# Optimization experiments

Measured on AMD Instinct MI355X. Metric: run time of the kernel, lower is better.

Reference implementation:

```python
import jax, jax.numpy as jnp
import numpy as np

H, D = 6, 64          # num_heads, head_dim (embed_dim = 384)
WIN = 33              # window_size
PAD = (WIN - 1) // 2  # 16


def setup_inputs() -> dict:
    key = jax.random.key(0)
    ks = jax.random.split(key, 9)
    B, L, E = 8, 1025, 384
    s = 1.0 / np.sqrt(E).astype(np.float32)
    return {
        "x": jax.random.normal(ks[0], (B, L, E), jnp.float32),
        "Wq": jax.random.normal(ks[1], (E, E), jnp.float32) * s,
        "bq": jax.random.normal(ks[2], (E,), jnp.float32) * 0.01,
        "Wk": jax.random.normal(ks[3], (E, E), jnp.float32) * s,
        "bk": jax.random.normal(ks[4], (E,), jnp.float32) * 0.01,
        "Wv": jax.random.normal(ks[5], (E, E), jnp.float32) * s,
        "bv": jax.random.normal(ks[6], (E,), jnp.float32) * 0.01,
        "Wo": jax.random.normal(ks[7], (E, E), jnp.float32) * s,
        "bo": jax.random.normal(ks[8], (E,), jnp.float32) * 0.01,
    }


def reference(x, Wq, bq, Wk, bk, Wv, bv, Wo, bo):
    B, L, E = x.shape
    scale = 1.0 / np.sqrt(D).astype(np.float32)

    def proj(W, b):
        # (B,L,E) -> (B,H,L,D)
        return (x @ W + b).reshape(B, L, H, D).transpose(0, 2, 1, 3)

    Q, K, V = proj(Wq, bq), proj(Wk, bk), proj(Wv, bv)

    # --- cls token (position 0): full attention over all keys ---
    s_cls = jnp.einsum('bhqd,bhkd->bhqk', Q[:, :, :1], K) * scale
    out_cls = jnp.einsum('bhqk,bhkd->bhqd', jax.nn.softmax(s_cls, -1), V)

    # --- remaining tokens: local window + cls appended to every window ---
    Lr = L - 1
    pos = jnp.arange(1, L)                                    # absolute query pos (Lr,)
    idx = pos[:, None] + jnp.arange(WIN)[None, :] - PAD
    # original masks out-of-range AND the cls slot (abs pos 0) inside the window
    valid = (idx >= 1) & (idx < L)
    idxc = jnp.clip(idx, 0, L - 1)

    Kw = K[:, :, idxc]
    Vw = V[:, :, idxc]
    cls_k = jnp.broadcast_to(K[:, :, :1, None, :], (B, H, Lr, 1, D))
    cls_v = jnp.broadcast_to(V[:, :, :1, None, :], (B, H, Lr, 1, D))
    Kw = jnp.concatenate([Kw, cls_k], axis=3)
    Vw = jnp.concatenate([Vw, cls_v], axis=3)
    mask = jnp.concatenate([valid, jnp.ones((Lr, 1), bool)], axis=-1)

    s_rest = jnp.einsum('bhld,bhlwd->bhlw', Q[:, :, 1:], Kw) * scale
    s_rest = jnp.where(mask[None, None], s_rest, -jnp.inf)
    a_rest = jax.nn.softmax(s_rest, axis=-1)
    out_rest = jnp.einsum('bhlw,bhlwd->bhld', a_rest, Vw)

    out = jnp.concatenate([out_cls, out_rest], axis=2)        # (B,H,L,D)
    out = out.transpose(0, 2, 1, 3).reshape(B, L, E)
    return out @ Wo + bo
```

## Files before the change

kernel.cpp:

```cpp
#include <hip/hip_runtime.h>
#include <hip/hip_bf16.h>

typedef unsigned short ushort_t;
typedef __attribute__((ext_vector_type(8))) short short8;
typedef __attribute__((ext_vector_type(4))) float f32x4;

constexpr int Bc = 8;
constexpr int Lc = 1025;
constexpr int Ec = 384;
constexpr int Hc = 6;
constexpr int Dc = 64;
constexpr int MT = Bc * Lc;
constexpr int BHLD = Bc * Hc * Lc * Dc;
constexpr float SCALE = 0.125f;
constexpr int NCH = 5;

__device__ __forceinline__ float bf2f(ushort_t u) {
    union { unsigned int u; float f; } v; v.u = ((unsigned int)u) << 16; return v.f;
}
__device__ __forceinline__ ushort_t f2bf(float f) {
    union { float f; unsigned int u; } v; v.f = f;
    unsigned int r = v.u + 0x7FFFu + ((v.u >> 16) & 1u);
    return (ushort_t)(r >> 16);
}

#define GLOAD_LDS16(gp, lp)                                                          \
    __builtin_amdgcn_global_load_lds(                                                \
        (const __attribute__((address_space(1))) unsigned int*)(gp),                 \
        (__attribute__((address_space(3))) unsigned int*)(lp), 16, 0, 0)

__global__ __launch_bounds__(256) void prep_kernel(
    const float* __restrict__ x, ushort_t* __restrict__ xb,
    const float* __restrict__ Wq, const float* __restrict__ Wk,
    const float* __restrict__ Wv, const float* __restrict__ Wo,
    ushort_t* __restrict__ Wt_all)
{
    const int bid = blockIdx.x;
    if (bid < 3075) {
        int i = bid * 256 + threadIdx.x;
        float4 v = ((const float4*)x)[i];
        ushort4 o;
        o.x = f2bf(v.x); o.y = f2bf(v.y); o.z = f2bf(v.z); o.w = f2bf(v.w);
        ((ushort4*)xb)[i] = o;
        return;
    }
    __shared__ float t[32][33];
    const int b2 = bid - 3075;
    const int z = b2 / 144, rem = b2 - z * 144;
    const int yy = rem / 12, xx = rem - yy * 12;
    const float* W = (z == 0) ? Wq : (z == 1) ? Wk : (z == 2) ? Wv : Wo;
    ushort_t* Wt = Wt_all + (size_t)z * Ec * Ec;
    const int x0 = xx * 32, y0 = yy * 32;
    const int tx = threadIdx.x & 31, ty = threadIdx.x >> 5;
#pragma unroll
    for (int j = 0; j < 4; j++)
        t[ty + 8 * j][tx] = W[(size_t)(y0 + ty + 8 * j) * Ec + x0 + tx];
    __syncthreads();
#pragma unroll
    for (int j = 0; j < 4; j++)
        Wt[(size_t)(x0 + ty + 8 * j) * Ec + y0 + tx] = f2bf(t[tx][ty + 8 * j]);
}

__global__ __launch_bounds__(256) void qkv_mfma_kernel(
    const ushort_t* __restrict__ xb, const ushort_t* __restrict__ Wt,
    const float* __restrict__ bq, const float* __restrict__ bk,
    const float* __restrict__ bv, ushort_t* __restrict__ qkv)
{
    __shared__ __align__(16) ushort_t As[128 * 64];
    __shared__ __align__(16) ushort_t Bs[128 * 64];

    const int tid = threadIdx.x;
    const int lane = tid & 63;
    const int wid = tid >> 6;
    const int wr = wid >> 1, wc = wid & 1;
    const int m0 = blockIdx.x * 128;
    const int n0 = blockIdx.y * 128;
    const int which = n0 / Ec;
    const int nm0 = n0 - which * Ec;
    const ushort_t* Wmat = Wt + (size_t)which * Ec * Ec;
    const float* bias = (which == 0) ? bq : (which == 1) ? bk : bv;

    f32x4 acc[4][4];
#pragma unroll
    for (int i = 0; i < 4; i++)
#pragma unroll
        for (int j = 0; j < 4; j++) acc[i][j] = (f32x4){0.f, 0.f, 0.f, 0.f};

    for (int kt = 0; kt < Ec; kt += 64) {
#pragma unroll
        for (int c = 0; c < 4; c++) {
            int ci  = (wid * 4 + c) * 64 + lane;
            int row = ci >> 3, kc = ci & 7;
            int kcs = kc ^ (row & 7);
            int rowA = m0 + row; rowA = rowA < MT ? rowA : MT - 1;
            GLOAD_LDS16(xb + (size_t)rowA * Ec + kt + kcs * 8,
                        As + (size_t)(wid * 4 + c) * 512);
            GLOAD_LDS16(Wmat + (size_t)(nm0 + row) * Ec + kt + kcs * 8,
                        Bs + (size_t)(wid * 4 + c) * 512);
        }
        __syncthreads();

#pragma unroll
        for (int ki = 0; ki < 2; ki++) {
            short8 a[4], b[4];
            const int kchunk = ki * 4 + (lane >> 4);
#pragma unroll
            for (int mi = 0; mi < 4; mi++) {
                int row = wr * 64 + mi * 16 + (lane & 15);
                a[mi] = *(const short8*)(As + row * 64 + ((kchunk ^ (row & 7)) * 8));
            }
#pragma unroll
            for (int ni = 0; ni < 4; ni++) {
                int row = wc * 64 + ni * 16 + (lane & 15);
                b[ni] = *(const short8*)(Bs + row * 64 + ((kchunk ^ (row & 7)) * 8));
            }
#pragma unroll
            for (int mi = 0; mi < 4; mi++)
#pragma unroll
                for (int ni = 0; ni < 4; ni++)
                    acc[mi][ni] = __builtin_amdgcn_mfma_f32_16x16x32_bf16(
                        a[mi], b[ni], acc[mi][ni], 0, 0, 0);
        }
        __syncthreads();
    }

    const int colL = lane & 15;
    const int rowL = (lane >> 4) * 4;
#pragma unroll
    for (int ni = 0; ni < 4; ni++) {
        int nm = nm0 + wc * 64 + ni * 16 + colL;
        float bv_ = bias[nm];
        int h = nm >> 6, d = nm & 63;
#pragma unroll
        for (int mi = 0; mi < 4; mi++) {
#pragma unroll
            for (int r = 0; r < 4; r++) {
                int m = m0 + wr * 64 + mi * 16 + rowL + r;
                if (m < MT) {
                    int b_ = m / Lc, l = m - b_ * Lc;
                    qkv[(size_t)which * BHLD +
                        ((size_t)(b_ * Hc + h) * Lc + l) * Dc + d] =
                        f2bf(acc[mi][ni][r] + bv_);
                }
            }
        }
    }
}

__global__ __launch_bounds__(256) void cls_part_kernel(
    const ushort_t* __restrict__ qkv, float* __restrict__ part)
{
    const int bh = blockIdx.x, ch = blockIdx.y;
    const int base = ch * 256;
    const int count = min(256, Lc - base);
    const ushort_t* Q = qkv + (size_t)bh * Lc * Dc;
    const ushort_t* K = Q + (size_t)BHLD;
    const ushort_t* V = Q + 2 * (size_t)BHLD;

    __shared__ float qs[64];
    __shared__ float ps[256];
    __shared__ float red[256];

    const int tid = threadIdx.x;
    if (tid < 64) qs[tid] = bf2f(Q[tid]);
    __syncthreads();

    float s = -1e30f;
    if (tid < count) {
        const ushort4* kp = (const ushort4*)(K + (size_t)(base + tid) * Dc);
        float acc = 0.f;
#pragma unroll
        for (int c = 0; c < 16; c++) {
            ushort4 kv = kp[c];
            acc += qs[c * 4 + 0] * bf2f(kv.x) + qs[c * 4 + 1] * bf2f(kv.y) +
                   qs[c * 4 + 2] * bf2f(kv.z) + qs[c * 4 + 3] * bf2f(kv.w);
        }
        s = acc * SCALE;
    }
    red[tid] = s; __syncthreads();
    for (int off = 128; off > 0; off >>= 1) {
        if (tid < off) red[tid] = fmaxf(red[tid], red[tid + off]);
        __syncthreads();
    }
    const float m = red[0];
    __syncthreads();

    float p = (tid < count) ? __expf(s - m) : 0.f;
    ps[tid] = p;
    red[tid] = p; __syncthreads();
    for (int off = 128; off > 0; off >>= 1) {
        if (tid < off) red[tid] += red[tid + off];
        __syncthreads();
    }
    const float S = red[0];
    __syncthreads();

    const int d = tid & 63, sl = tid >> 6;
    float acc = 0.f;
    for (int i = sl; i < count; i += 4)
        acc += ps[i] * bf2f(V[(size_t)(base + i) * Dc + d]);
    red[tid] = acc; __syncthreads();
    if (tid < 64) {
        float o = red[tid] + red[tid + 64] + red[tid + 128] + red[tid + 192];
        float* pp = part + (size_t)(bh * NCH + ch) * 66;
        pp[2 + tid] = o;
        if (tid == 0) { pp[0] = m; pp[1] = S; }
    }
}

__global__ __launch_bounds__(256) void win_attn_kernel(
    const ushort_t* __restrict__ qkv, const float* __restrict__ part,
    ushort_t* __restrict__ attnb)
{
    __shared__ __align__(16) ushort_t Kb[128 * 64];
    __shared__ __align__(16) ushort_t Vb[64 * 128];
    __shared__ __align__(16) ushort_t QP[64 * 128];

    const int bh = blockIdx.y;
    const int tid = threadIdx.x, lane = tid & 63, wid = tid >> 6;
    const int b_ = bh / Hc, h = bh - b_ * Hc;

    if (blockIdx.x == 16) {
        if (tid >= 64) return;
        float M = -1e30f;
#pragma unroll
        for (int ch = 0; ch < NCH; ch++)
            M = fmaxf(M, part[(size_t)(bh * NCH + ch) * 66]);
        float S = 0.f, O = 0.f;
#pragma unroll
        for (int ch = 0; ch < NCH; ch++) {
            const float* pp = part + (size_t)(bh * NCH + ch) * 66;
            float w = __expf(pp[0] - M);
            S += pp[1] * w;
            O += pp[2 + tid] * w;
        }
        attnb[(size_t)(b_ * Lc) * Ec + h * 64 + tid] = f2bf(O / S);
        return;
    }

    const int t = blockIdx.x;
    const int l0 = 1 + t * 64;
    const int k0n = l0 - 16;
    const ushort_t* Qg = qkv + (size_t)bh * Lc * Dc;
    const ushort_t* Kg = Qg + (size_t)BHLD;
    const ushort_t* Vg = Qg + 2 * (size_t)BHLD;

    short8 vreg[4];
    int vrow[4], vdc[4];
#pragma unroll
    for (int i = 0; i < 4; i++) {
        int ci = i * 256 + tid;
        if (ci < 896) {
            int j = ci >> 3, dc = ci & 7;
            int kp = (j <= 95) ? min(max(k0n + j, 0), 1024) : 0;
            vreg[i] = *(const short8*)(Vg + (size_t)kp * Dc + dc * 8);
            vrow[i] = j; vdc[i] = dc;
        } else { vrow[i] = -1; vdc[i] = 0; }
    }

#pragma unroll
    for (int i = 0; i < 4; i++) {
        int wchunk = i * 4 + wid;
        if (wchunk < 14) {
            int p = wchunk * 64 + lane;
            int j = p >> 3, c = p & 7, g = c ^ (j & 7);
            int kp = (j <= 95) ? min(max(k0n + j, 0), 1024) : 0;
            GLOAD_LDS16(Kg + (size_t)kp * Dc + g * 8,
                        Kb + (size_t)wchunk * 512);
        }
    }
#pragma unroll
    for (int i = 0; i < 2; i++) {
        int p = (i * 4 + wid) * 64 + lane;
        int q = p >> 3, c = p & 7, g = c ^ (q & 7);
        GLOAD_LDS16(Qg + (size_t)(l0 + q) * Dc + g * 8,
                    QP + (size_t)(i * 4 + wid) * 512);
    }

#pragma unroll
    for (int i = 0; i < 4; i++) {
        if (vrow[i] >= 0) {
            int j = vrow[i], jc3 = j >> 3, j7 = j & 7;
#pragma unroll
            for (int z = 0; z < 8; z++) {
                int d = vdc[i] * 8 + z;
                Vb[d * 128 + ((jc3 ^ (d & 15)) * 8) + j7] = (ushort_t)vreg[i][z];
            }
        }
    }
    if (tid < 128) {
        int d = tid >> 1, lcn = 14 + (tid & 1);
        *(short8*)(Vb + d * 128 + ((lcn ^ (d & 15)) * 8)) =
            (short8){0, 0, 0, 0, 0, 0, 0, 0};
    }
    __syncthreads();

    f32x4 sacc[7];
#pragma unroll
    for (int tj = 0; tj < 7; tj++) sacc[tj] = (f32x4){0.f, 0.f, 0.f, 0.f};
#pragma unroll
    for (int ki = 0; ki < 2; ki++) {
        const int gc = ki * 4 + (lane >> 4);
        const int qrow = wid * 16 + (lane & 15);
        short8 a = *(const short8*)(QP + qrow * 64 + ((gc ^ (qrow & 7)) * 8));
#pragma unroll
        for (int tj = 0; tj < 7; tj++) {
            int jrow = tj * 16 + (lane & 15);
            short8 b = *(const short8*)(Kb + jrow * 64 + ((gc ^ (jrow & 7)) * 8));
            sacc[tj] = __builtin_amdgcn_mfma_f32_16x16x32_bf16(a, b, sacc[tj], 0, 0, 0);
        }
    }
    __syncthreads();

    const int qb = wid * 16 + (lane >> 4) * 4;
    const int cl = lane & 15;
    float inv[4];
#pragma unroll
    for (int r = 0; r < 4; r++) {
        const int q = qb + r;
        float sv[7];
        float mx = -1e30f;
#pragma unroll
        for (int tj = 0; tj < 7; tj++) {
            int j = tj * 16 + cl;
            int kp = k0n + j;
            bool valid = (j == 96) ||
                         ((j >= q) && (j <= q + 32) && (kp >= 1) && (kp <= 1024));
            float s = valid ? sacc[tj][r] * SCALE : -1e30f;
            sv[tj] = s;
            mx = fmaxf(mx, s);
        }
        mx = fmaxf(mx, __shfl_xor(mx, 1));
        mx = fmaxf(mx, __shfl_xor(mx, 2));
        mx = fmaxf(mx, __shfl_xor(mx, 4));
        mx = fmaxf(mx, __shfl_xor(mx, 8));
        float sum = 0.f;
#pragma unroll
        for (int tj = 0; tj < 7; tj++) {
            float pv = __expf(sv[tj] - mx);
            sv[tj] = pv;
            sum += pv;
        }
        sum += __shfl_xor(sum, 1);
        sum += __shfl_xor(sum, 2);
        sum += __shfl_xor(sum, 4);
        sum += __shfl_xor(sum, 8);
        inv[r] = 1.f / sum;
#pragma unroll
        for (int tj = 0; tj < 7; tj++) {
            int j = tj * 16 + cl;
            QP[q * 128 + (((j >> 3) ^ (q & 15)) * 8) + (j & 7)] = f2bf(sv[tj]);
        }
    }
    if (cl == 0) {
#pragma unroll
        for (int r = 0; r < 4; r++) {
            int q = qb + r;
            *(short8*)(QP + q * 128 + ((14 ^ (q & 15)) * 8)) =
                (short8){0, 0, 0, 0, 0, 0, 0, 0};
            *(short8*)(QP + q * 128 + ((15 ^ (q & 15)) * 8)) =
                (short8){0, 0, 0, 0, 0, 0, 0, 0};
        }
    }
    __syncthreads();

    f32x4 oacc[4];
#pragma unroll
    for (int dt = 0; dt < 4; dt++) oacc[dt] = (f32x4){0.f, 0.f, 0.f, 0.f};
#pragma unroll
    for (int kc = 0; kc < 4; kc++) {
        const int gc = kc * 4 + (lane >> 4);
        const int qrow = wid * 16 + (lane & 15);
        short8 pa = *(const short8*)(QP + qrow * 128 + ((gc ^ (qrow & 15)) * 8));
#pragma unroll
        for (int dt = 0; dt < 4; dt++) {
            int drow = dt * 16 + (lane & 15);
            short8 vb = *(const short8*)(Vb + drow * 128 + ((gc ^ (drow & 15)) * 8));
            oacc[dt] = __builtin_amdgcn_mfma_f32_16x16x32_bf16(pa, vb, oacc[dt], 0, 0, 0);
        }
    }

#pragma unroll
    for (int dt = 0; dt < 4; dt++) {
        int d = dt * 16 + cl;
#pragma unroll
        for (int r = 0; r < 4; r++) {
            int l = l0 + qb + r;
            attnb[(size_t)(b_ * Lc + l) * Ec + h * 64 + d] = f2bf(oacc[dt][r] * inv[r]);
        }
    }
}

__global__ __launch_bounds__(256) void out_mfma_kernel(
    const ushort_t* __restrict__ attn_rows, const ushort_t* __restrict__ Wot,
    const float* __restrict__ bo, float* __restrict__ out)
{
    __shared__ __align__(16) ushort_t As[64 * 64];
    __shared__ __align__(16) ushort_t Bs[128 * 64];

    const int tid = threadIdx.x;
    const int lane = tid & 63;
    const int wid = tid >> 6;
    const int wr = wid & 1, wc = wid >> 1;
    const int m0 = blockIdx.x * 64;
    const int n0 = blockIdx.y * 128;

    f32x4 acc[2][4];
#pragma unroll
    for (int i = 0; i < 2; i++)
#pragma unroll
        for (int j = 0; j < 4; j++) acc[i][j] = (f32x4){0.f, 0.f, 0.f, 0.f};

    for (int kt = 0; kt < Ec; kt += 64) {
#pragma unroll
        for (int c = 0; c < 2; c++) {
            int ci  = (wid * 2 + c) * 64 + lane;
            int row = ci >> 3, kc = ci & 7;
            int kcs = kc ^ (row & 7);
            int rowA = m0 + row; rowA = rowA < MT ? rowA : MT - 1;
            GLOAD_LDS16(attn_rows + (size_t)rowA * Ec + kt + kcs * 8,
                        As + (size_t)(wid * 2 + c) * 512);
        }
#pragma unroll
        for (int c = 0; c < 4; c++) {
            int ci  = (wid * 4 + c) * 64 + lane;
            int row = ci >> 3, kc = ci & 7;
            int kcs = kc ^ (row & 7);
            GLOAD_LDS16(Wot + (size_t)(n0 + row) * Ec + kt + kcs * 8,
                        Bs + (size_t)(wid * 4 + c) * 512);
        }
        __syncthreads();

#pragma unroll
        for (int ki = 0; ki < 2; ki++) {
            short8 a[2], b[4];
            const int kchunk = ki * 4 + (lane >> 4);
#pragma unroll
            for (int mi = 0; mi < 2; mi++) {
                int row = wr * 32 + mi * 16 + (lane & 15);
                a[mi] = *(const short8*)(As + row * 64 + ((kchunk ^ (row & 7)) * 8));
            }
#pragma unroll
            for (int ni = 0; ni < 4; ni++) {
                int row = wc * 64 + ni * 16 + (lane & 15);
                b[ni] = *(const short8*)(Bs + row * 64 + ((kchunk ^ (row & 7)) * 8));
            }
#pragma unroll
            for (int mi = 0; mi < 2; mi++)
#pragma unroll
                for (int ni = 0; ni < 4; ni++)
                    acc[mi][ni] = __builtin_amdgcn_mfma_f32_16x16x32_bf16(
                        a[mi], b[ni], acc[mi][ni], 0, 0, 0);
        }
        __syncthreads();
    }

    const int colL = lane & 15;
    const int rowL = (lane >> 4) * 4;
#pragma unroll
    for (int ni = 0; ni < 4; ni++) {
        int n = n0 + wc * 64 + ni * 16 + colL;
        float bo_v = bo[n];
#pragma unroll
        for (int mi = 0; mi < 2; mi++) {
#pragma unroll
            for (int r = 0; r < 4; r++) {
                int m = m0 + wr * 32 + mi * 16 + rowL + r;
                if (m < MT) out[(size_t)m * Ec + n] = acc[mi][ni][r] + bo_v;
            }
        }
    }
}

extern "C" void kernel_launch(void* const* d_in, const int* in_sizes, int n_in,
                              void* d_out, int out_size, void* d_ws, size_t ws_size,
                              hipStream_t stream)
{
    const float* x  = (const float*)d_in[0];
    const float* Wq = (const float*)d_in[1];
    const float* bq = (const float*)d_in[2];
    const float* Wk = (const float*)d_in[3];
    const float* bk = (const float*)d_in[4];
    const float* Wv = (const float*)d_in[5];
    const float* bv = (const float*)d_in[6];
    const float* Wo = (const float*)d_in[7];
    const float* bo = (const float*)d_in[8];
    float* out = (float*)d_out;

    ushort_t* xb    = (ushort_t*)d_ws;
    ushort_t* Wt    = xb + (size_t)MT * Ec;
    ushort_t* qkvb  = Wt + (size_t)4 * Ec * Ec;
    ushort_t* attnb = qkvb + (size_t)3 * BHLD;
    float* clsp     = (float*)(attnb + (size_t)MT * Ec);

    prep_kernel<<<3075 + 576, 256, 0, stream>>>(x, xb, Wq, Wk, Wv, Wo, Wt);

    qkv_mfma_kernel<<<dim3((MT + 127) / 128, 9), 256, 0, stream>>>(
        xb, Wt, bq, bk, bv, qkvb);

    cls_part_kernel<<<dim3(Bc * Hc, NCH), 256, 0, stream>>>(qkvb, clsp);

    win_attn_kernel<<<dim3(17, Bc * Hc), 256, 0, stream>>>(qkvb, clsp, attnb);

    out_mfma_kernel<<<dim3((MT + 63) / 64, 3), 256, 0, stream>>>(
        attnb, Wt + (size_t)3 * Ec * Ec, bo, out);
}
```

Before: 163.9 us.

## Double-buffer LDS tiles in QKV and output projection GEMMs

```diff
diff --git a/kernel.cpp b/kernel.cpp
--- a/kernel.cpp
+++ b/kernel.cpp
@@ -66,8 +66,8 @@
     const float* __restrict__ bq, const float* __restrict__ bk,
     const float* __restrict__ bv, ushort_t* __restrict__ qkv)
 {
-    __shared__ __align__(16) ushort_t As[128 * 64];
-    __shared__ __align__(16) ushort_t Bs[128 * 64];
+    __shared__ __align__(16) ushort_t As[2][128 * 64];
+    __shared__ __align__(16) ushort_t Bs[2][128 * 64];
 
     const int tid = threadIdx.x;
     const int lane = tid & 63;
@@ -86,43 +86,62 @@
 #pragma unroll
         for (int j = 0; j < 4; j++) acc[i][j] = (f32x4){0.f, 0.f, 0.f, 0.f};
 
-    for (int kt = 0; kt < Ec; kt += 64) {
-#pragma unroll
-        for (int c = 0; c < 4; c++) {
-            int ci  = (wid * 4 + c) * 64 + lane;
-            int row = ci >> 3, kc = ci & 7;
-            int kcs = kc ^ (row & 7);
-            int rowA = m0 + row; rowA = rowA < MT ? rowA : MT - 1;
-            GLOAD_LDS16(xb + (size_t)rowA * Ec + kt + kcs * 8,
-                        As + (size_t)(wid * 4 + c) * 512);
-            GLOAD_LDS16(Wmat + (size_t)(nm0 + row) * Ec + kt + kcs * 8,
-                        Bs + (size_t)(wid * 4 + c) * 512);
-        }
-        __syncthreads();
-
+#define QKV_STAGE(KT, BUF)                                                       \
+    {                                                                            \
+        _Pragma("unroll")                                                        \
+        for (int c = 0; c < 4; c++) {                                            \
+            int ci  = (wid * 4 + c) * 64 + lane;                                 \
+            int row = ci >> 3, kc = ci & 7;                                      \
+            int kcs = kc ^ (row & 7);                                            \
+            int rowA = m0 + row; rowA = rowA < MT ? rowA : MT - 1;               \
+            GLOAD_LDS16(xb + (size_t)rowA * Ec + (KT) + kcs * 8,                 \
+                        As[BUF] + (size_t)(wid * 4 + c) * 512);                  \
+            GLOAD_LDS16(Wmat + (size_t)(nm0 + row) * Ec + (KT) + kcs * 8,        \
+                        Bs[BUF] + (size_t)(wid * 4 + c) * 512);                  \
+        }                                                                        \
+    }
+
+    QKV_STAGE(0, 0);
+    QKV_STAGE(64, 1);
+
+    for (int t = 0; t < 6; ++t) {
+        const int cb = t & 1;
+        if (t < 5) { asm volatile("s_waitcnt vmcnt(8)" ::: "memory"); }
+        else       { asm volatile("s_waitcnt vmcnt(0)" ::: "memory"); }
+        __builtin_amdgcn_sched_barrier(0);
+        __builtin_amdgcn_s_barrier();
+
+        short8 a[2][4], b[2][4];
 #pragma unroll
         for (int ki = 0; ki < 2; ki++) {
-            short8 a[4], b[4];
             const int kchunk = ki * 4 + (lane >> 4);
 #pragma unroll
             for (int mi = 0; mi < 4; mi++) {
                 int row = wr * 64 + mi * 16 + (lane & 15);
-                a[mi] = *(const short8*)(As + row * 64 + ((kchunk ^ (row & 7)) * 8));
+                a[ki][mi] = *(const short8*)(As[cb] + row * 64 + ((kchunk ^ (row & 7)) * 8));
             }
 #pragma unroll
             for (int ni = 0; ni < 4; ni++) {
                 int row = wc * 64 + ni * 16 + (lane & 15);
-                b[ni] = *(const short8*)(Bs + row * 64 + ((kchunk ^ (row & 7)) * 8));
-            }
+                b[ki][ni] = *(const short8*)(Bs[cb] + row * 64 + ((kchunk ^ (row & 7)) * 8));
+            }
+        }
+        asm volatile("s_waitcnt lgkmcnt(0)" ::: "memory");
+        __builtin_amdgcn_sched_barrier(0);
+        __builtin_amdgcn_s_barrier();
+
+        if (t + 2 < 6) QKV_STAGE((t + 2) * 64, cb);
+
+#pragma unroll
+        for (int ki = 0; ki < 2; ki++)
 #pragma unroll
             for (int mi = 0; mi < 4; mi++)
 #pragma unroll
                 for (int ni = 0; ni < 4; ni++)
                     acc[mi][ni] = __builtin_amdgcn_mfma_f32_16x16x32_bf16(
-                        a[mi], b[ni], acc[mi][ni], 0, 0, 0);
-        }
-        __syncthreads();
-    }
+                        a[ki][mi], b[ki][ni], acc[mi][ni], 0, 0, 0);
+    }
+#undef QKV_STAGE
 
     const int colL = lane & 15;
     const int rowL = (lane >> 4) * 4;
@@ -395,8 +414,8 @@
     const ushort_t* __restrict__ attn_rows, const ushort_t* __restrict__ Wot,
     const float* __restrict__ bo, float* __restrict__ out)
 {
-    __shared__ __align__(16) ushort_t As[64 * 64];
-    __shared__ __align__(16) ushort_t Bs[128 * 64];
+    __shared__ __align__(16) ushort_t As[2][64 * 64];
+    __shared__ __align__(16) ushort_t Bs[2][128 * 64];
 
     const int tid = threadIdx.x;
     const int lane = tid & 63;
@@ -411,49 +430,68 @@
 #pragma unroll
         for (int j = 0; j < 4; j++) acc[i][j] = (f32x4){0.f, 0.f, 0.f, 0.f};
 
-    for (int kt = 0; kt < Ec; kt += 64) {
-#pragma unroll
-        for (int c = 0; c < 2; c++) {
-            int ci  = (wid * 2 + c) * 64 + lane;
-            int row = ci >> 3, kc = ci & 7;
-            int kcs = kc ^ (row & 7);
-            int rowA = m0 + row; rowA = rowA < MT ? rowA : MT - 1;
-            GLOAD_LDS16(attn_rows + (size_t)rowA * Ec + kt + kcs * 8,
-                        As + (size_t)(wid * 2 + c) * 512);
-        }
-#pragma unroll
-        for (int c = 0; c < 4; c++) {
-            int ci  = (wid * 4 + c) * 64 + lane;
-            int row = ci >> 3, kc = ci & 7;
-            int kcs = kc ^ (row & 7);
-            GLOAD_LDS16(Wot + (size_t)(n0 + row) * Ec + kt + kcs * 8,
-                        Bs + (size_t)(wid * 4 + c) * 512);
-        }
-        __syncthreads();
-
+#define OUT_STAGE(KT, BUF)                                                       \
+    {                                                                            \
+        _Pragma("unroll")                                                        \
+        for (int c = 0; c < 2; c++) {                                            \
+            int ci  = (wid * 2 + c) * 64 + lane;                                 \
+            int row = ci >> 3, kc = ci & 7;                                      \
+            int kcs = kc ^ (row & 7);                                            \
+            int rowA = m0 + row; rowA = rowA < MT ? rowA : MT - 1;               \
+            GLOAD_LDS16(attn_rows + (size_t)rowA * Ec + (KT) + kcs * 8,          \
+                        As[BUF] + (size_t)(wid * 2 + c) * 512);                  \
+        }                                                                        \
+        _Pragma("unroll")                                                        \
+        for (int c = 0; c < 4; c++) {                                            \
+            int ci  = (wid * 4 + c) * 64 + lane;                                 \
+            int row = ci >> 3, kc = ci & 7;                                      \
+            int kcs = kc ^ (row & 7);                                            \
+            GLOAD_LDS16(Wot + (size_t)(n0 + row) * Ec + (KT) + kcs * 8,          \
+                        Bs[BUF] + (size_t)(wid * 4 + c) * 512);                  \
+        }                                                                        \
+    }
+
+    OUT_STAGE(0, 0);
+    OUT_STAGE(64, 1);
+
+    for (int t = 0; t < 6; ++t) {
+        const int cb = t & 1;
+        if (t < 5) { asm volatile("s_waitcnt vmcnt(6)" ::: "memory"); }
+        else       { asm volatile("s_waitcnt vmcnt(0)" ::: "memory"); }
+        __builtin_amdgcn_sched_barrier(0);
+        __builtin_amdgcn_s_barrier();
+
+        short8 a[2][2], b[2][4];
 #pragma unroll
         for (int ki = 0; ki < 2; ki++) {
-            short8 a[2], b[4];
             const int kchunk = ki * 4 + (lane >> 4);
 #pragma unroll
             for (int mi = 0; mi < 2; mi++) {
                 int row = wr * 32 + mi * 16 + (lane & 15);
-                a[mi] = *(const short8*)(As + row * 64 + ((kchunk ^ (row & 7)) * 8));
+                a[ki][mi] = *(const short8*)(As[cb] + row * 64 + ((kchunk ^ (row & 7)) * 8));
             }
 #pragma unroll
             for (int ni = 0; ni < 4; ni++) {
                 int row = wc * 64 + ni * 16 + (lane & 15);
-                b[ni] = *(const short8*)(Bs + row * 64 + ((kchunk ^ (row & 7)) * 8));
-            }
+                b[ki][ni] = *(const short8*)(Bs[cb] + row * 64 + ((kchunk ^ (row & 7)) * 8));
+            }
+        }
+        asm volatile("s_waitcnt lgkmcnt(0)" ::: "memory");
+        __builtin_amdgcn_sched_barrier(0);
+        __builtin_amdgcn_s_barrier();
+
+        if (t + 2 < 6) OUT_STAGE((t + 2) * 64, cb);
+
+#pragma unroll
+        for (int ki = 0; ki < 2; ki++)
 #pragma unroll
             for (int mi = 0; mi < 2; mi++)
 #pragma unroll
                 for (int ni = 0; ni < 4; ni++)
                     acc[mi][ni] = __builtin_amdgcn_mfma_f32_16x16x32_bf16(
-                        a[mi], b[ni], acc[mi][ni], 0, 0, 0);
-        }
-        __syncthreads();
-    }
+                        a[ki][mi], b[ki][ni], acc[mi][ni], 0, 0, 0);
+    }
+#undef OUT_STAGE
 
     const int colL = lane & 15;
     const int rowL = (lane >> 4) * 4;
```

Result: faster. 160.3 us (-2.2%).
